# Kernel optimization log

Hardware: AMD Instinct MI355X
Metric: run time of the kernel (lower is better)

The kernel has to match this reference:

```python
import jax, jax.numpy as jnp
import numpy as np

_TWO_PI_3 = 2.0 * np.pi / 3.0
_EPS = 1e-7


def _eig3_sym(y, m):
    """Closed-form ascending eigenvalues of per-voxel 3x3 symmetric tensors.

    y: [B,6,H,W,D] scaled+masked channels (xx,xy,xz,yy,yz,zz); m: [B,H,W,D] mask.
    Masked-out voxels (m==0) are replaced by diag(1,2,3) so the solve is
    non-degenerate everywhere; they carry zero weight in the loss so the
    forward value is unchanged.
    """
    pad = 1.0 - m
    a00 = y[:, 0] + pad
    a01 = y[:, 1]
    a02 = y[:, 2]
    a11 = y[:, 3] + 2.0 * pad
    a12 = y[:, 4]
    a22 = y[:, 5] + 3.0 * pad
    q = (a00 + a11 + a22) / 3.0
    p2 = (a00 - q) ** 2 + (a11 - q) ** 2 + (a22 - q) ** 2 + 2.0 * (a01 ** 2 + a02 ** 2 + a12 ** 2)
    p = jnp.sqrt(p2 / 6.0)
    ps = jnp.where(p > 0, p, 1.0)
    b00 = (a00 - q) / ps
    b11 = (a11 - q) / ps
    b22 = (a22 - q) / ps
    b01 = a01 / ps
    b02 = a02 / ps
    b12 = a12 / ps
    det_b = (b00 * (b11 * b22 - b12 * b12)
             - b01 * (b01 * b22 - b12 * b02)
             + b02 * (b01 * b12 - b11 * b02))
    r = jnp.clip(0.5 * det_b, -1.0 + _EPS, 1.0 - _EPS)
    phi = jnp.arccos(r) / 3.0
    l2 = q + 2.0 * p * jnp.cos(phi)            # largest
    l0 = q + 2.0 * p * jnp.cos(phi + _TWO_PI_3)  # smallest
    l1 = 3.0 * q - l0 - l2
    return l0, l1, l2


def setup_inputs() -> dict:
    key = jax.random.key(0)
    k1, k2, k3, k4, k5 = jax.random.split(key, 5)
    B, H, W, D = 4, 96, 96, 96
    input_data = jax.random.normal(k1, (B, 6, H, W, D), jnp.float32)
    target = jax.random.normal(k2, (B, 6, H, W, D), jnp.float32)
    mask = jax.random.randint(k3, (B, 1, H, W, D), 0, 2, jnp.int32)
    gt_mean = jax.random.normal(k4, (6, 1, 1, 1), jnp.float32)
    gt_std = jax.random.uniform(k5, (6, 1, 1, 1), jnp.float32) + 0.5
    return {"input_data": input_data, "target": target, "mask": mask,
            "gt_mean": gt_mean, "gt_std": gt_std}


def reference(input_data, target, mask, gt_mean, gt_std):
    mask_f = mask.astype(jnp.float32)            # [B,1,H,W,D]
    m = mask_f[:, 0]                             # [B,H,W,D]
    scale = gt_std[None]                         # [1,6,1,1,1]
    shift = gt_mean[None]
    new_input = (input_data * scale + shift) * mask_f
    new_target = (target * scale + shift) * mask_f
    i0, i1, i2 = _eig3_sym(new_input, m)
    t0, t1, _t2 = _eig3_sym(new_target, m)
    input_ani = i2 - 0.5 * (i0 + i1)
    # NOTE: replicates the original's chained assignment bug:
    # target_ani = target_eigval[:, 2] = 0.5 * (l0 + l1)
    target_ani = 0.5 * (t0 + t1)
    n = jnp.maximum(jnp.sum(m), 1.0)
    loss = jnp.sum(jnp.abs(input_ani - target_ani) * m) / n
    return loss
```

## Files before the change

### kernel.cpp

```cpp
#include <hip/hip_runtime.h>


namespace {
constexpr int SB    = 96 * 96 * 96;
constexpr int BATCH = 4;
constexpr int NVOX  = SB * BATCH;
constexpr int N4    = NVOX / 4;
constexpr int BLOCK = 256;
constexpr int GRID  = N4 / BLOCK;
constexpr int BLOCK2 = 1024;

__device__ __forceinline__ float f4get(const float4& v, int j) {
    return ((const float*)&v)[j];
}

__device__ __forceinline__ float eig_pc(const float y0, const float y1, const float y2,
                                        const float y3, const float y4, const float y5,
                                        float& q_out) {
    const float q  = (y0 + y3 + y5) * (1.0f / 3.0f);
    const float d0 = y0 - q, d1 = y3 - q, d2 = y5 - q;
    float p2 = d0 * d0;
    p2 = fmaf(d1, d1, p2);
    p2 = fmaf(d2, d2, p2);
    float c2 = y1 * y1;
    c2 = fmaf(y2, y2, c2);
    c2 = fmaf(y4, y4, c2);
    p2 = fmaf(2.0f, c2, p2);
    const float p2s = p2 * (1.0f / 6.0f);
    const float inv = rsqrtf(fmaxf(p2s, 1e-12f));
    const float p   = p2s * inv;

    const float m0 = fmaf(d1, d2, -(y4 * y4));
    const float m1 = fmaf(y1, d2, -(y4 * y2));
    const float m2 = fmaf(y1, y4, -(d1 * y2));
    float det = d0 * m0;
    det = fmaf(-y1, m1, det);
    det = fmaf( y2, m2, det);

    float r = 0.5f * det * (inv * inv * inv);
    r = fminf(fmaxf(r, -1.0f + 1e-7f), 1.0f - 1e-7f);

    const float a  = fabsf(r);
    const float sq = sqrtf(1.0f - a);
    float poly = fmaf(a, -0.0187293f, 0.0742610f);
    poly = fmaf(a, poly, -0.2121144f);
    poly = fmaf(a, poly, 1.5707288f);
    const float t  = sq * poly;
    const float th = (r < 0.0f) ? (3.14159265358979f - t) : t;
    const float phi = th * (1.0f / 3.0f);

    const float u = phi * phi;
    float c = fmaf(u, 2.4801587e-5f, -1.3888889e-3f);
    c = fmaf(u, c, 4.16666679e-2f);
    c = fmaf(u, c, -0.5f);
    c = fmaf(u, c, 1.0f);

    q_out = q;
    return p * c;
}

__global__ __launch_bounds__(BLOCK) void ani_reduce(
    const float* __restrict__ in, const float* __restrict__ tg,
    const int*  __restrict__ mask,
    const float* __restrict__ gt_mean, const float* __restrict__ gt_std,
    float* __restrict__ ws) {

    float st[6], mn[6];
#pragma unroll
    for (int c = 0; c < 6; ++c) { st[c] = gt_std[c]; mn[c] = gt_mean[c]; }

    float sum_abs = 0.0f;
    float sum_m   = 0.0f;

    int i = blockIdx.x * blockDim.x + threadIdx.x;
    {
        int v4 = i * 4;
        int b  = v4 / SB;
        int s  = v4 - b * SB;
        int base = (b * 6) * SB + s;

        float4 xi[6], xt[6];
#pragma unroll
        for (int c = 0; c < 6; ++c) {
            xi[c] = *(const float4*)(in + base + c * SB);
            xt[c] = *(const float4*)(tg + base + c * SB);
        }
        int4 mk = *(const int4*)(mask + b * SB + s);
        int mks[4] = {mk.x, mk.y, mk.z, mk.w};

#pragma unroll
        for (int j = 0; j < 4; ++j) {
            float mf = (float)mks[j];
            float yi[6], yt[6];
#pragma unroll
            for (int c = 0; c < 6; ++c) {
                yi[c] = fmaf(f4get(xi[c], j), st[c], mn[c]);
                yt[c] = fmaf(f4get(xt[c], j), st[c], mn[c]);
            }
            float qi, qt;
            float pci = eig_pc(yi[0], yi[1], yi[2], yi[3], yi[4], yi[5], qi);
            float pct = eig_pc(yt[0], yt[1], yt[2], yt[3], yt[4], yt[5], qt);
            float ani_in = 3.0f * pci;
            float ani_tg = qt - pct;
            sum_abs = fmaf(fabsf(ani_in - ani_tg), mf, sum_abs);
            sum_m  += mf;
        }
    }

#pragma unroll
    for (int off = 32; off > 0; off >>= 1) {
        sum_abs += __shfl_down(sum_abs, off, 64);
        sum_m   += __shfl_down(sum_m,   off, 64);
    }
    __shared__ float s_abs[BLOCK / 64];
    __shared__ float s_m[BLOCK / 64];
    int lane = threadIdx.x & 63;
    int wid  = threadIdx.x >> 6;
    if (lane == 0) { s_abs[wid] = sum_abs; s_m[wid] = sum_m; }
    __syncthreads();
    if (threadIdx.x == 0) {
        float ta = 0.0f, tm = 0.0f;
#pragma unroll
        for (int w = 0; w < BLOCK / 64; ++w) { ta += s_abs[w]; tm += s_m[w]; }
        ws[blockIdx.x]        = ta;
        ws[GRID + blockIdx.x] = tm;
    }
}

__global__ __launch_bounds__(BLOCK2) void ani_stage2(
    const float* __restrict__ ws, float* __restrict__ out) {
    float sa = 0.0f, sm = 0.0f;
    for (int i = threadIdx.x; i < GRID; i += BLOCK2) {
        sa += ws[i];
        sm += ws[GRID + i];
    }
#pragma unroll
    for (int off = 32; off > 0; off >>= 1) {
        sa += __shfl_down(sa, off, 64);
        sm += __shfl_down(sm, off, 64);
    }
    __shared__ float s_abs[BLOCK2 / 64];
    __shared__ float s_m[BLOCK2 / 64];
    int lane = threadIdx.x & 63;
    int wid  = threadIdx.x >> 6;
    if (lane == 0) { s_abs[wid] = sa; s_m[wid] = sm; }
    __syncthreads();
    if (threadIdx.x == 0) {
        float ta = 0.0f, tm = 0.0f;
#pragma unroll
        for (int w = 0; w < BLOCK2 / 64; ++w) { ta += s_abs[w]; tm += s_m[w]; }
        out[0] = ta / fmaxf(tm, 1.0f);
    }
}

}

extern "C" void kernel_launch(void* const* d_in, const int* in_sizes, int n_in,
                              void* d_out, int out_size, void* d_ws, size_t ws_size,
                              hipStream_t stream) {
    const float* in      = (const float*)d_in[0];
    const float* tg      = (const float*)d_in[1];
    const int*   mask    = (const int*)d_in[2];
    const float* gt_mean = (const float*)d_in[3];
    const float* gt_std  = (const float*)d_in[4];
    float* ws  = (float*)d_ws;
    float* out = (float*)d_out;

    ani_reduce<<<GRID, BLOCK, 0, stream>>>(in, tg, mask, gt_mean, gt_std, ws);
    ani_stage2<<<1, BLOCK2, 0, stream>>>(ws, out);
}
```

Before: 199.3 us.

## Process four float4 chunks per thread with double-buffered register prefetch

Each thread now handles four 4-voxel chunks instead of one, shrinking the grid by four. Before computing the current chunk it issues the loads for the next one into a second register buffer, so memory latency overlaps with the eigenvalue arithmetic. This also cuts the number of block-level reductions and stage-2 inputs. The cost is roughly double the register use for the staged inputs, which may lower occupancy.

```diff
diff --git a/kernel.cpp b/kernel.cpp
--- a/kernel.cpp
+++ b/kernel.cpp
@@ -7,7 +7,8 @@
 constexpr int NVOX  = SB * BATCH;
 constexpr int N4    = NVOX / 4;
 constexpr int BLOCK = 256;
-constexpr int GRID  = N4 / BLOCK;
+constexpr int ITER  = 4;
+constexpr int GRID  = N4 / (BLOCK * ITER);
 constexpr int BLOCK2 = 1024;
 
 __device__ __forceinline__ float f4get(const float4& v, int j) {
@@ -72,30 +73,51 @@
     float sum_abs = 0.0f;
     float sum_m   = 0.0f;
 
-    int i = blockIdx.x * blockDim.x + threadIdx.x;
+    const int g0 = blockIdx.x * (BLOCK * ITER) + threadIdx.x;
+
+    float4 xi[2][6], xt[2][6];
+    int4   mk[2];
+
     {
-        int v4 = i * 4;
+        int v4 = g0 * 4;
         int b  = v4 / SB;
         int s  = v4 - b * SB;
         int base = (b * 6) * SB + s;
-
-        float4 xi[6], xt[6];
 #pragma unroll
         for (int c = 0; c < 6; ++c) {
-            xi[c] = *(const float4*)(in + base + c * SB);
-            xt[c] = *(const float4*)(tg + base + c * SB);
+            xi[0][c] = *(const float4*)(in + base + c * SB);
+            xt[0][c] = *(const float4*)(tg + base + c * SB);
         }
-        int4 mk = *(const int4*)(mask + b * SB + s);
-        int mks[4] = {mk.x, mk.y, mk.z, mk.w};
+        mk[0] = *(const int4*)(mask + b * SB + s);
+    }
 
+#pragma unroll
+    for (int it = 0; it < ITER; ++it) {
+        const int cur = it & 1;
+        const int nxt = cur ^ 1;
+        if (it + 1 < ITER) {
+            int g  = g0 + (it + 1) * BLOCK;
+            int v4 = g * 4;
+            int b  = v4 / SB;
+            int s  = v4 - b * SB;
+            int base = (b * 6) * SB + s;
+#pragma unroll
+            for (int c = 0; c < 6; ++c) {
+                xi[nxt][c] = *(const float4*)(in + base + c * SB);
+                xt[nxt][c] = *(const float4*)(tg + base + c * SB);
+            }
+            mk[nxt] = *(const int4*)(mask + b * SB + s);
+        }
+
+        int mks[4] = {mk[cur].x, mk[cur].y, mk[cur].z, mk[cur].w};
 #pragma unroll
         for (int j = 0; j < 4; ++j) {
             float mf = (float)mks[j];
             float yi[6], yt[6];
 #pragma unroll
             for (int c = 0; c < 6; ++c) {
-                yi[c] = fmaf(f4get(xi[c], j), st[c], mn[c]);
-                yt[c] = fmaf(f4get(xt[c], j), st[c], mn[c]);
+                yi[c] = fmaf(f4get(xi[cur][c], j), st[c], mn[c]);
+                yt[c] = fmaf(f4get(xt[cur][c], j), st[c], mn[c]);
             }
             float qi, qt;
             float pci = eig_pc(yi[0], yi[1], yi[2], yi[3], yi[4], yi[5], qi);
```

New measurement: 204.8 us. 1.03x slower.
